# Kernel tuning notes

Hardware: AMD Instinct MI355X
Metric: run time of the kernel (lower is better)

The kernel has to match this reference:

```python
import jax, jax.numpy as jnp
import numpy as np


def setup_inputs() -> dict:
    key = jax.random.key(0)
    k1, k2 = jax.random.split(key)
    B, N, M = 8, 8192, 8192
    xyz1 = jax.random.normal(k1, (B, N, 3), dtype=jnp.float32)
    xyz2 = jax.random.normal(k2, (B, M, 3), dtype=jnp.float32)
    return {"xyz1": xyz1, "xyz2": xyz2}


def reference(xyz1, xyz2):
    x2 = jnp.sum(xyz1 * xyz1, axis=-1)  # [B, N]
    y2 = jnp.sum(xyz2 * xyz2, axis=-1)  # [B, M]
    xy = jnp.einsum("bnd,bmd->bnm", xyz1, xyz2)  # [B, N, M]
    d = x2[:, :, None] + y2[:, None, :] - 2.0 * xy
    dist1 = jnp.min(d, axis=2)  # nearest neighbor of each point in xyz1 -> [B, N]
    dist2 = jnp.min(d, axis=1)  # nearest neighbor of each point in xyz2 -> [B, M]
    return jnp.mean(dist1) + jnp.mean(dist2)
```

## Files before the change

### kernel.cpp

```cpp
#include <hip/hip_runtime.h>


typedef float  f32x16 __attribute__((ext_vector_type(16)));
typedef __bf16 bf16x8 __attribute__((ext_vector_type(8)));

constexpr int B  = 8;
constexpr int N  = 8192;
constexpr int BN = B * N;
constexpr int NQ = 2 * BN;
constexpr int CO = 4;

__device__ inline ushort f2bh(float x) {
  unsigned u = __float_as_uint(x);
  return (ushort)((u + 0x7FFFu + ((u >> 16) & 1u)) >> 16);
}
__device__ inline float bh2f(ushort h) { return __uint_as_float(((unsigned)h) << 16); }

__global__ __launch_bounds__(256) void pack_both_kernel(
    const float* __restrict__ xyz1, const float* __restrict__ xyz2,
    ushort* __restrict__ kvA1, ushort* __restrict__ kvB1,
    ushort* __restrict__ kvA2, ushort* __restrict__ kvB2) {
  int i = blockIdx.x * 256 + threadIdx.x;
  bool s1 = i < BN;
  const float* src = s1 ? xyz1 : xyz2;
  ushort* kvA = s1 ? kvA1 : kvA2;
  ushort* kvB = s1 ? kvB1 : kvB2;
  int j = s1 ? i : i - BN;
  float x = src[3 * j], y = src[3 * j + 1], z = src[3 * j + 2];
  float w = fmaf(x, x, fmaf(y, y, z * z));
  ushort xh = f2bh(x), yh = f2bh(y), zh = f2bh(z), wh = f2bh(w);
  ushort xl = f2bh(x - bh2f(xh)), yl = f2bh(y - bh2f(yh));
  ushort zl = f2bh(z - bh2f(zh)), wl = f2bh(w - bh2f(wh));
  const unsigned ONE2 = 0x3F803F80u;
  unsigned pw = (unsigned)wh | ((unsigned)wl << 16);
  {
    ushort axh = f2bh(-2.f * bh2f(xh)), axl = f2bh(-2.f * bh2f(xl));
    ushort ayh = f2bh(-2.f * bh2f(yh)), ayl = f2bh(-2.f * bh2f(yl));
    ushort azh = f2bh(-2.f * bh2f(zh)), azl = f2bh(-2.f * bh2f(zl));
    unsigned px = (unsigned)axh | ((unsigned)axl << 16);
    unsigned py = (unsigned)ayh | ((unsigned)ayl << 16);
    unsigned pz = (unsigned)azh | ((unsigned)azl << 16);
    *(uint4*)(kvA + (size_t)j * 16)     = make_uint4(px, px, py, py);
    *(uint4*)(kvA + (size_t)j * 16 + 8) = make_uint4(pz, pz, pw, ONE2);
  }
  {
    unsigned bx0 = (unsigned)xh | ((unsigned)xh << 16);
    unsigned bx1 = (unsigned)xl | ((unsigned)xl << 16);
    unsigned by0 = (unsigned)yh | ((unsigned)yh << 16);
    unsigned by1 = (unsigned)yl | ((unsigned)yl << 16);
    unsigned bz0 = (unsigned)zh | ((unsigned)zh << 16);
    unsigned bz1 = (unsigned)zl | ((unsigned)zl << 16);
    *(uint4*)(kvB + (size_t)j * 16)     = make_uint4(bx0, bx1, by0, by1);
    *(uint4*)(kvB + (size_t)j * 16 + 8) = make_uint4(bz0, bz1, ONE2, pw);
  }
}

__global__ __launch_bounds__(256, 2) void nn_mfma32_kernel(
    const ushort* __restrict__ kvA1, const ushort* __restrict__ kvB1,
    const ushort* __restrict__ kvA2, const ushort* __restrict__ kvB2,
    float* __restrict__ part) {
  __shared__ __align__(16) unsigned char smem[1024 * 32];
  ushort* kb = (ushort*)smem;
  float (*red)[32][36] = (float (*)[32][36])smem;

  const int bid = blockIdx.x;
  const int qg  = bid & 31;
  const int c   = (bid >> 5) & 3;
  const int b   = (bid >> 7) & 7;
  const int dir = (bid >> 10) & 1;
  const ushort* __restrict__ kvA = dir ? kvA2 : kvA1;
  const ushort* __restrict__ kvB = dir ? kvB1 : kvB2;

  const int tid = threadIdx.x;
  const int w = tid >> 6, lane = tid & 63;
  const int cl = lane & 31, hi = lane >> 5;

  const int qbase = b * N + qg * 256 + w * 64;
  bf16x8 af[2];
  #pragma unroll
  for (int a = 0; a < 2; ++a)
    af[a] = *(const bf16x8*)(kvA + (size_t)(qbase + a * 32 + cl) * 16 + hi * 8);

  float rmin[2][16];
  #pragma unroll
  for (int a = 0; a < 2; ++a)
    #pragma unroll
    for (int r = 0; r < 16; ++r) rmin[a][r] = 3.4e38f;

  const f32x16 cz = {0.f, 0.f, 0.f, 0.f, 0.f, 0.f, 0.f, 0.f,
                     0.f, 0.f, 0.f, 0.f, 0.f, 0.f, 0.f, 0.f};
  const int tbase = b * N + c * 2048;

  #pragma unroll 1
  for (int half = 0; half < 2; ++half) {
    if (half) __syncthreads();
    {
      const uint4* src = (const uint4*)(kvB + (size_t)(tbase + half * 1024) * 16);
      uint4* dst = (uint4*)kb;
      #pragma unroll
      for (int i = 0; i < 8; ++i) dst[tid + i * 256] = src[tid + i * 256];
    }
    __syncthreads();

    #pragma unroll 1
    for (int jp = 0; jp < 16; ++jp) {
      const ushort* kp = kb + (jp * 64 + cl) * 16 + hi * 8;
      bf16x8 bf0 = *(const bf16x8*)(kp);
      bf16x8 bf1 = *(const bf16x8*)(kp + 32 * 16);
      #pragma unroll
      for (int a = 0; a < 2; ++a) {
        f32x16 acc0 = __builtin_amdgcn_mfma_f32_32x32x16_bf16(af[a], bf0, cz, 0, 0, 0);
        f32x16 acc1 = __builtin_amdgcn_mfma_f32_32x32x16_bf16(af[a], bf1, cz, 0, 0, 0);
        #pragma unroll
        for (int r = 0; r < 16; ++r)
          rmin[a][r] = fminf(rmin[a][r], fminf(acc0[r], acc1[r]));
      }
    }
  }

  #pragma unroll
  for (int a = 0; a < 2; ++a) {
    __syncthreads();
    #pragma unroll
    for (int r = 0; r < 16; ++r) {
      int row = (r & 3) + 8 * (r >> 2) + 4 * hi;
      red[w][row][cl] = rmin[a][r];
    }
    __syncthreads();
    if (lane < 32) {
      float m = 3.4e38f;
      #pragma unroll
      for (int i = 0; i < 8; ++i) {
        float4 v = *(const float4*)&red[w][lane][i * 4];
        m = fminf(m, fminf(fminf(v.x, v.y), fminf(v.z, v.w)));
      }
      part[(size_t)c * NQ + dir * BN + qbase + a * 32 + lane] = m;
    }
  }
}

__global__ __launch_bounds__(256) void reduce_final_kernel(
    const float* __restrict__ part, float* __restrict__ blocksums) {
  int gq = blockIdx.x * 256 + threadIdx.x;
  float v = part[gq];
  #pragma unroll
  for (int cc = 1; cc < CO; ++cc) v = fminf(v, part[(size_t)cc * NQ + gq]);
  #pragma unroll
  for (int off = 32; off > 0; off >>= 1) v += __shfl_down(v, off);
  __shared__ float ssum[4];
  const int lane = threadIdx.x & 63, wid = threadIdx.x >> 6;
  if (lane == 0) ssum[wid] = v;
  __syncthreads();
  if (threadIdx.x == 0)
    blocksums[blockIdx.x] = ssum[0] + ssum[1] + ssum[2] + ssum[3];
}

__global__ __launch_bounds__(512) void finalize_sums_kernel(
    const float* __restrict__ blocksums, float* __restrict__ out) {
  float v = blocksums[threadIdx.x];
  #pragma unroll
  for (int off = 32; off > 0; off >>= 1) v += __shfl_down(v, off);
  __shared__ float ssum[8];
  const int lane = threadIdx.x & 63, wid = threadIdx.x >> 6;
  if (lane == 0) ssum[wid] = v;
  __syncthreads();
  if (threadIdx.x == 0) {
    float s = 0.f;
    #pragma unroll
    for (int w = 0; w < 8; ++w) s += ssum[w];
    out[0] = s * (1.0f / 65536.0f);
  }
}

__global__ __launch_bounds__(256) void pack4_kernel(
    const float* __restrict__ xyz1, const float* __restrict__ xyz2,
    float4* __restrict__ p1, float4* __restrict__ p2) {
  int i = blockIdx.x * 256 + threadIdx.x;
  const float* s = (i < BN) ? xyz1 : xyz2;
  float4* d      = (i < BN) ? p1 : p2;
  int j          = (i < BN) ? i : (i - BN);
  float x = s[3 * j], y = s[3 * j + 1], z = s[3 * j + 2];
  d[j] = make_float4(x, y, z, fmaf(x, x, fmaf(y, y, z * z)));
}

__global__ __launch_bounds__(256) void nn_packed_kernel(
    const float4* __restrict__ p1, const float4* __restrict__ p2,
    float* __restrict__ blocksums) {
  const int bid   = blockIdx.x;
  const int dir   = bid >> 8;
  const int idx   = bid & 255;
  const int b     = idx >> 5;
  const int chunk = idx & 31;
  const float4* __restrict__ q = (dir ? p2 : p1) + b * N + chunk * 256;
  const float4* __restrict__ t = (dir ? p1 : p2) + b * N;

  float4 qv = q[threadIdx.x];
  const float qx = -2.0f * qv.x, qy = -2.0f * qv.y, qz = -2.0f * qv.z;

  float mn0 = 3.4e38f, mn1 = 3.4e38f, mn2 = 3.4e38f, mn3 = 3.4e38f;
  #pragma unroll 2
  for (int m = 0; m < N; m += 4) {
    float4 t0 = t[m + 0], t1 = t[m + 1], t2 = t[m + 2], t3 = t[m + 3];
    float d0 = fmaf(qx, t0.x, fmaf(qy, t0.y, fmaf(qz, t0.z, t0.w)));
    float d1 = fmaf(qx, t1.x, fmaf(qy, t1.y, fmaf(qz, t1.z, t1.w)));
    float d2 = fmaf(qx, t2.x, fmaf(qy, t2.y, fmaf(qz, t2.z, t2.w)));
    float d3 = fmaf(qx, t3.x, fmaf(qy, t3.y, fmaf(qz, t3.z, t3.w)));
    mn0 = fminf(mn0, d0); mn1 = fminf(mn1, d1);
    mn2 = fminf(mn2, d2); mn3 = fminf(mn3, d3);
  }
  float v = qv.w + fminf(fminf(mn0, mn1), fminf(mn2, mn3));

  #pragma unroll
  for (int off = 32; off > 0; off >>= 1) v += __shfl_down(v, off);
  __shared__ float ssum[4];
  const int lane = threadIdx.x & 63, wid = threadIdx.x >> 6;
  if (lane == 0) ssum[wid] = v;
  __syncthreads();
  if (threadIdx.x == 0)
    blocksums[bid] = ssum[0] + ssum[1] + ssum[2] + ssum[3];
}

extern "C" void kernel_launch(void* const* d_in, const int* in_sizes, int n_in,
                              void* d_out, int out_size, void* d_ws, size_t ws_size,
                              hipStream_t stream) {
  const float* xyz1 = (const float*)d_in[0];
  const float* xyz2 = (const float*)d_in[1];
  float* out = (float*)d_out;

  ushort* kvA1 = (ushort*)d_ws;
  ushort* kvB1 = kvA1 + (size_t)BN * 16;
  ushort* kvA2 = kvB1 + (size_t)BN * 16;
  ushort* kvB2 = kvA2 + (size_t)BN * 16;
  float* part = (float*)(kvB2 + (size_t)BN * 16);
  float* blocksums = part + (size_t)CO * NQ;
  const size_t need = (size_t)BN * 16 * 2 * 4 + (size_t)CO * NQ * 4 +
                      512 * sizeof(float);

  if (ws_size >= need) {
    pack_both_kernel<<<(2 * BN) / 256, 256, 0, stream>>>(
        xyz1, xyz2, kvA1, kvB1, kvA2, kvB2);
    nn_mfma32_kernel<<<2048, 256, 0, stream>>>(kvA1, kvB1, kvA2, kvB2, part);
    reduce_final_kernel<<<NQ / 256, 256, 0, stream>>>(part, blocksums);
    finalize_sums_kernel<<<1, 512, 0, stream>>>(blocksums, out);
  } else {
    float4* p1 = (float4*)d_ws;
    float4* p2 = p1 + BN;
    float* bsum = (float*)(p2 + BN);
    pack4_kernel<<<(2 * BN) / 256, 256, 0, stream>>>(xyz1, xyz2, p1, p2);
    nn_packed_kernel<<<512, 256, 0, stream>>>(p1, p2, bsum);
    finalize_sums_kernel<<<1, 512, 0, stream>>>(bsum, out);
  }
}
```

Before: 49.19 us.

## Replace partial-min buffer with atomicMin and fuse final reduction via atomics

```diff
diff --git a/kernel.cpp b/kernel.cpp
--- a/kernel.cpp
+++ b/kernel.cpp
@@ -8,7 +8,6 @@
 constexpr int N  = 8192;
 constexpr int BN = B * N;
 constexpr int NQ = 2 * BN;
-constexpr int CO = 4;
 
 __device__ inline ushort f2bh(float x) {
   unsigned u = __float_as_uint(x);
@@ -19,8 +18,11 @@
 __global__ __launch_bounds__(256) void pack_both_kernel(
     const float* __restrict__ xyz1, const float* __restrict__ xyz2,
     ushort* __restrict__ kvA1, ushort* __restrict__ kvB1,
-    ushort* __restrict__ kvA2, ushort* __restrict__ kvB2) {
+    ushort* __restrict__ kvA2, ushort* __restrict__ kvB2,
+    unsigned* __restrict__ pmin, unsigned long long* __restrict__ acc) {
   int i = blockIdx.x * 256 + threadIdx.x;
+  pmin[i] = 0xFFFFFFFFu;
+  if (i == 0) { acc[0] = 0ull; acc[1] = 0ull; }
   bool s1 = i < BN;
   const float* src = s1 ? xyz1 : xyz2;
   ushort* kvA = s1 ? kvA1 : kvA2;
@@ -58,7 +60,7 @@
 __global__ __launch_bounds__(256, 2) void nn_mfma32_kernel(
     const ushort* __restrict__ kvA1, const ushort* __restrict__ kvB1,
     const ushort* __restrict__ kvA2, const ushort* __restrict__ kvB2,
-    float* __restrict__ part) {
+    unsigned* __restrict__ pmin) {
   __shared__ __align__(16) unsigned char smem[1024 * 32];
   ushort* kb = (ushort*)smem;
   float (*red)[32][36] = (float (*)[32][36])smem;
@@ -134,17 +136,78 @@
         float4 v = *(const float4*)&red[w][lane][i * 4];
         m = fminf(m, fminf(fminf(v.x, v.y), fminf(v.z, v.w)));
       }
-      part[(size_t)c * NQ + dir * BN + qbase + a * 32 + lane] = m;
-    }
-  }
-}
-
-__global__ __launch_bounds__(256) void reduce_final_kernel(
-    const float* __restrict__ part, float* __restrict__ blocksums) {
+      unsigned u = __float_as_uint(m);
+      u = (u & 0x80000000u) ? ~u : (u | 0x80000000u);
+      atomicMin(&pmin[dir * BN + qbase + a * 32 + lane], u);
+    }
+  }
+}
+
+__global__ __launch_bounds__(256) void reduce_sum_kernel(
+    const unsigned* __restrict__ pmin, unsigned long long* __restrict__ acc,
+    float* __restrict__ out) {
   int gq = blockIdx.x * 256 + threadIdx.x;
-  float v = part[gq];
-  #pragma unroll
-  for (int cc = 1; cc < CO; ++cc) v = fminf(v, part[(size_t)cc * NQ + gq]);
+  unsigned k = pmin[gq];
+  float v = __uint_as_float((k & 0x80000000u) ? (k & 0x7FFFFFFFu) : ~k);
+  #pragma unroll
+  for (int off = 32; off > 0; off >>= 1) v += __shfl_down(v, off);
+  __shared__ float ssum[4];
+  const int lane = threadIdx.x & 63, wid = threadIdx.x >> 6;
+  if (lane == 0) ssum[wid] = v;
+  __syncthreads();
+  if (threadIdx.x == 0) {
+    double s = (double)ssum[0] + (double)ssum[1] +
+               (double)ssum[2] + (double)ssum[3];
+    long long q = (long long)(s * 4294967296.0);
+    atomicAdd(&acc[0], (unsigned long long)q);
+    __threadfence();
+    unsigned long long t = atomicAdd(&acc[1], 1ull);
+    if (t == (unsigned long long)(gridDim.x - 1)) {
+      unsigned long long total = atomicAdd(&acc[0], 0ull);
+      double tot = (double)(long long)total * (1.0 / 4294967296.0);
+      out[0] = (float)(tot * (1.0 / 65536.0));
+    }
+  }
+}
+
+__global__ __launch_bounds__(256) void pack4_kernel(
+    const float* __restrict__ xyz1, const float* __restrict__ xyz2,
+    float4* __restrict__ p1, float4* __restrict__ p2) {
+  int i = blockIdx.x * 256 + threadIdx.x;
+  const float* s = (i < BN) ? xyz1 : xyz2;
+  float4* d      = (i < BN) ? p1 : p2;
+  int j          = (i < BN) ? i : (i - BN);
+  float x = s[3 * j], y = s[3 * j + 1], z = s[3 * j + 2];
+  d[j] = make_float4(x, y, z, fmaf(x, x, fmaf(y, y, z * z)));
+}
+
+__global__ __launch_bounds__(256) void nn_packed_kernel(
+    const float4* __restrict__ p1, const float4* __restrict__ p2,
+    float* __restrict__ blocksums) {
+  const int bid   = blockIdx.x;
+  const int dir   = bid >> 8;
+  const int idx   = bid & 255;
+  const int b     = idx >> 5;
+  const int chunk = idx & 31;
+  const float4* __restrict__ q = (dir ? p2 : p1) + b * N + chunk * 256;
+  const float4* __restrict__ t = (dir ? p1 : p2) + b * N;
+
+  float4 qv = q[threadIdx.x];
+  const float qx = -2.0f * qv.x, qy = -2.0f * qv.y, qz = -2.0f * qv.z;
+
+  float mn0 = 3.4e38f, mn1 = 3.4e38f, mn2 = 3.4e38f, mn3 = 3.4e38f;
+  #pragma unroll 2
+  for (int m = 0; m < N; m += 4) {
+    float4 t0 = t[m + 0], t1 = t[m + 1], t2 = t[m + 2], t3 = t[m + 3];
+    float d0 = fmaf(qx, t0.x, fmaf(qy, t0.y, fmaf(qz, t0.z, t0.w)));
+    float d1 = fmaf(qx, t1.x, fmaf(qy, t1.y, fmaf(qz, t1.z, t1.w)));
+    float d2 = fmaf(qx, t2.x, fmaf(qy, t2.y, fmaf(qz, t2.z, t2.w)));
+    float d3 = fmaf(qx, t3.x, fmaf(qy, t3.y, fmaf(qz, t3.z, t3.w)));
+    mn0 = fminf(mn0, d0); mn1 = fminf(mn1, d1);
+    mn2 = fminf(mn2, d2); mn3 = fminf(mn3, d3);
+  }
+  float v = qv.w + fminf(fminf(mn0, mn1), fminf(mn2, mn3));
+
   #pragma unroll
   for (int off = 32; off > 0; off >>= 1) v += __shfl_down(v, off);
   __shared__ float ssum[4];
@@ -152,7 +215,7 @@
   if (lane == 0) ssum[wid] = v;
   __syncthreads();
   if (threadIdx.x == 0)
-    blocksums[blockIdx.x] = ssum[0] + ssum[1] + ssum[2] + ssum[3];
+    blocksums[bid] = ssum[0] + ssum[1] + ssum[2] + ssum[3];
 }
 
 __global__ __launch_bounds__(512) void finalize_sums_kernel(
@@ -172,54 +235,6 @@
   }
 }
 
-__global__ __launch_bounds__(256) void pack4_kernel(
-    const float* __restrict__ xyz1, const float* __restrict__ xyz2,
-    float4* __restrict__ p1, float4* __restrict__ p2) {
-  int i = blockIdx.x * 256 + threadIdx.x;
-  const float* s = (i < BN) ? xyz1 : xyz2;
-  float4* d      = (i < BN) ? p1 : p2;
-  int j          = (i < BN) ? i : (i - BN);
-  float x = s[3 * j], y = s[3 * j + 1], z = s[3 * j + 2];
-  d[j] = make_float4(x, y, z, fmaf(x, x, fmaf(y, y, z * z)));
-}
-
-__global__ __launch_bounds__(256) void nn_packed_kernel(
-    const float4* __restrict__ p1, const float4* __restrict__ p2,
-    float* __restrict__ blocksums) {
-  const int bid   = blockIdx.x;
-  const int dir   = bid >> 8;
-  const int idx   = bid & 255;
-  const int b     = idx >> 5;
-  const int chunk = idx & 31;
-  const float4* __restrict__ q = (dir ? p2 : p1) + b * N + chunk * 256;
-  const float4* __restrict__ t = (dir ? p1 : p2) + b * N;
-
-  float4 qv = q[threadIdx.x];
-  const float qx = -2.0f * qv.x, qy = -2.0f * qv.y, qz = -2.0f * qv.z;
-
-  float mn0 = 3.4e38f, mn1 = 3.4e38f, mn2 = 3.4e38f, mn3 = 3.4e38f;
-  #pragma unroll 2
-  for (int m = 0; m < N; m += 4) {
-    float4 t0 = t[m + 0], t1 = t[m + 1], t2 = t[m + 2], t3 = t[m + 3];
-    float d0 = fmaf(qx, t0.x, fmaf(qy, t0.y, fmaf(qz, t0.z, t0.w)));
-    float d1 = fmaf(qx, t1.x, fmaf(qy, t1.y, fmaf(qz, t1.z, t1.w)));
-    float d2 = fmaf(qx, t2.x, fmaf(qy, t2.y, fmaf(qz, t2.z, t2.w)));
-    float d3 = fmaf(qx, t3.x, fmaf(qy, t3.y, fmaf(qz, t3.z, t3.w)));
-    mn0 = fminf(mn0, d0); mn1 = fminf(mn1, d1);
-    mn2 = fminf(mn2, d2); mn3 = fminf(mn3, d3);
-  }
-  float v = qv.w + fminf(fminf(mn0, mn1), fminf(mn2, mn3));
-
-  #pragma unroll
-  for (int off = 32; off > 0; off >>= 1) v += __shfl_down(v, off);
-  __shared__ float ssum[4];
-  const int lane = threadIdx.x & 63, wid = threadIdx.x >> 6;
-  if (lane == 0) ssum[wid] = v;
-  __syncthreads();
-  if (threadIdx.x == 0)
-    blocksums[bid] = ssum[0] + ssum[1] + ssum[2] + ssum[3];
-}
-
 extern "C" void kernel_launch(void* const* d_in, const int* in_sizes, int n_in,
                               void* d_out, int out_size, void* d_ws, size_t ws_size,
                               hipStream_t stream) {
@@ -231,17 +246,15 @@
   ushort* kvB1 = kvA1 + (size_t)BN * 16;
   ushort* kvA2 = kvB1 + (size_t)BN * 16;
   ushort* kvB2 = kvA2 + (size_t)BN * 16;
-  float* part = (float*)(kvB2 + (size_t)BN * 16);
-  float* blocksums = part + (size_t)CO * NQ;
-  const size_t need = (size_t)BN * 16 * 2 * 4 + (size_t)CO * NQ * 4 +
-                      512 * sizeof(float);
+  unsigned* pmin = (unsigned*)(kvB2 + (size_t)BN * 16);
+  unsigned long long* acc = (unsigned long long*)(pmin + NQ);
+  const size_t need = (size_t)BN * 16 * 2 * 4 + (size_t)NQ * 4 + 16;
 
   if (ws_size >= need) {
-    pack_both_kernel<<<(2 * BN) / 256, 256, 0, stream>>>(
-        xyz1, xyz2, kvA1, kvB1, kvA2, kvB2);
-    nn_mfma32_kernel<<<2048, 256, 0, stream>>>(kvA1, kvB1, kvA2, kvB2, part);
-    reduce_final_kernel<<<NQ / 256, 256, 0, stream>>>(part, blocksums);
-    finalize_sums_kernel<<<1, 512, 0, stream>>>(blocksums, out);
+    pack_both_kernel<<<NQ / 256, 256, 0, stream>>>(
+        xyz1, xyz2, kvA1, kvB1, kvA2, kvB2, pmin, acc);
+    nn_mfma32_kernel<<<2048, 256, 0, stream>>>(kvA1, kvB1, kvA2, kvB2, pmin);
+    reduce_sum_kernel<<<NQ / 256, 256, 0, stream>>>(pmin, acc, out);
   } else {
     float4* p1 = (float4*)d_ws;
     float4* p2 = p1 + BN;
```

After: 61.38 us. 24.8% more time.
